# Performance work log

Measured on AMD Instinct MI355X. Metric: run time of the kernel, lower is better.

## Reference

```python
import jax, jax.numpy as jnp
import numpy as np

# Static module config (from init_kwargs)
N, C, H, W = 2, 256, 64, 64
S = 2            # scale_factor
K = 5            # up_kernel
G = 1            # up_group
CC = 64          # compressed_channels
EK = 3           # encoder_kernel
HOUT, WOUT = H * S, W * S


def conv2d(x, w, b, pad):
    y = jax.lax.conv_general_dilated(
        x, w, window_strides=(1, 1), padding=[(pad, pad), (pad, pad)],
        dimension_numbers=('NCHW', 'OIHW', 'NCHW'))
    return y + b[None, :, None, None]


def grid_sample_border(img, gx, gy):
    """Bilinear grid_sample, padding_mode='border', align_corners=True.
    img: (N, Cm, Hh, Ww); gx, gy: (N, Hout, Wout) normalized coords in [-1,1]."""
    Hh, Ww = img.shape[2], img.shape[3]
    ix = jnp.clip((gx + 1.0) * 0.5 * (Ww - 1), 0.0, Ww - 1)
    iy = jnp.clip((gy + 1.0) * 0.5 * (Hh - 1), 0.0, Hh - 1)
    x0 = jnp.floor(ix)
    y0 = jnp.floor(iy)
    fx = ix - x0
    fy = iy - y0
    x0i = x0.astype(jnp.int32)
    y0i = y0.astype(jnp.int32)
    x1i = jnp.minimum(x0i + 1, Ww - 1)
    y1i = jnp.minimum(y0i + 1, Hh - 1)

    def per_n(im, x0n, x1n, y0n, y1n, fxn, fyn):
        v00 = im[:, y0n, x0n]   # (Cm, Hout, Wout)
        v01 = im[:, y0n, x1n]
        v10 = im[:, y1n, x0n]
        v11 = im[:, y1n, x1n]
        return (v00 * (1 - fxn) * (1 - fyn) + v01 * fxn * (1 - fyn)
                + v10 * (1 - fxn) * fyn + v11 * fxn * fyn)

    return jax.vmap(per_n)(img, x0i, x1i, y0i, y1i, fx, fy)


def setup_inputs() -> dict:
    key = jax.random.key(0)
    ks = jax.random.split(key, 8)
    x = jax.random.normal(ks[0], (N, C, H, W), dtype=jnp.float32)
    w_comp = jax.random.normal(ks[1], (CC, C, 1, 1), dtype=jnp.float32) * 0.05
    b_comp = jax.random.normal(ks[2], (CC,), dtype=jnp.float32) * 0.01
    # conv_offset is zero-init in the original; use small random weights to
    # exercise the deformable path.
    w_off = jax.random.normal(ks[3], (G * 2 * S * S, CC, EK, EK), dtype=jnp.float32) * 0.01
    b_off = jax.random.normal(ks[4], (G * 2 * S * S,), dtype=jnp.float32) * 0.01
    w_ker = jax.random.normal(ks[5], (K * K * G, CC, EK, EK), dtype=jnp.float32) * 0.01
    b_ker = jax.random.normal(ks[6], (K * K * G,), dtype=jnp.float32) * 0.01
    return {'x': x, 'w_comp': w_comp, 'b_comp': b_comp,
            'w_off': w_off, 'b_off': b_off, 'w_ker': w_ker, 'b_ker': b_ker}


def reference(x, w_comp, b_comp, w_off, b_off, w_ker, b_ker):
    # 1) channel compressor (1x1 conv)
    comp = conv2d(x, w_comp, b_comp, 0)                      # (N, CC, H, W)
    # 2) offset + kernel prediction (3x3 convs)
    off = conv2d(comp, w_off, b_off, (EK - 1) // 2)          # (N, 2*S*S*G, H, W)
    ker = conv2d(comp, w_ker, b_ker, (EK - 1) // 2)          # (N, G*K*K, H, W)
    # 3) kernel space normalizer: softmax over K*K per group
    m = ker.reshape(N, G, K * K, H, W)
    m = jax.nn.softmax(m, axis=2).reshape(N, G * K * K, H, W)
    # 4) kernel space expander: pixel_shuffle offset -> (N,2,HOUT,WOUT)
    o = off.reshape(N, 2, S, S, H, W).transpose(0, 1, 4, 2, 5, 3).reshape(N, 2, HOUT, WOUT)
    ox = o[:, 0] * (2.0 / (W - 1))   # x offset, normalized
    oy = o[:, 1] * (2.0 / (H - 1))   # y offset, normalized
    base_y = jnp.repeat(jnp.linspace(-1.0, 1.0, H), S)       # (HOUT,)
    base_x = jnp.repeat(jnp.linspace(-1.0, 1.0, W), S)       # (WOUT,)
    gx = base_x[None, None, :] + ox                          # (N, HOUT, WOUT)
    gy = base_y[None, :, None] + oy
    mask_up = grid_sample_border(m, gx, gy)                  # (N, G*K*K, HOUT, WOUT)
    # 5) CARAFE reassembly: unfold features at low res, weighted sum.
    pad = (K - 1) // 2
    xp = jnp.pad(x, ((0, 0), (0, 0), (pad, pad), (pad, pad)))
    unf = jnp.stack([xp[:, :, i:i + H, j:j + W]
                     for i in range(K) for j in range(K)], axis=2)  # (N,C,K*K,H,W)
    Cg = C // G
    unf = unf.reshape(N, G, Cg, K * K, H, W)
    # mask[..., h*S+p, w*S+q] selects low-res position (h, w): reshape instead
    # of materializing the (N,G,Cg,K*K,HOUT,WOUT) gathered tensor.
    mr = mask_up.reshape(N, G, K * K, H, S, W, S)
    out = jnp.einsum('ngckhw,ngkhpwq->ngchpwq', unf, mr)
    return out.reshape(N, C, HOUT, WOUT)
```

## Files before the change

### kernel.cpp

```cpp
#include <hip/hip_runtime.h>

#define NB 2
#define CIN 256
#define HH 64
#define WW 64
#define CCMP 64
#define HO 128
#define WO 128

#define CPLD 66
#define CPCH (CPLD * CPLD)
#define CPIMG (CCMP * CPCH)
#define CPTOT (NB * CPIMG)

#define OFF_OFFB  (CPTOT)
#define OFF_KERB  (OFF_OFFB + 65536)
#define OFF_WTS   (OFF_KERB + 204800)

__global__ __launch_bounds__(256) void k1_comp(const float* __restrict__ x,
                                               const float* __restrict__ wc,
                                               const float* __restrict__ bc,
                                               float* __restrict__ comp_pad) {
  int b = blockIdx.x;
  int n = b >> 8;
  int ccg = (b >> 4) & 15;
  int hq = b & 15;
  int hsub = threadIdx.x >> 6;
  int w = threadIdx.x & 63;
  int h = hq * 4 + hsub;

  float acc[4];
#pragma unroll
  for (int j = 0; j < 4; ++j) acc[j] = bc[ccg * 4 + j];
  const float* xp = x + ((size_t)(n * CIN) * HH + h) * WW + w;
#pragma unroll 4
  for (int c = 0; c < CIN; ++c) {
    float xv = xp[(size_t)c * HH * WW];
#pragma unroll
    for (int j = 0; j < 4; ++j) acc[j] += xv * wc[(ccg * 4 + j) * CIN + c];
  }
  float* plane = comp_pad + (size_t)n * CPIMG + (size_t)(ccg * 4) * CPCH;
#pragma unroll
  for (int j = 0; j < 4; ++j)
    plane[(size_t)j * CPCH + (h + 1) * CPLD + (w + 1)] = acc[j];

  if (threadIdx.x < 32) {
    int ch = threadIdx.x >> 3;
    int rw = (threadIdx.x >> 1) & 3;
    int side = threadIdx.x & 1;
    plane[(size_t)ch * CPCH + (hq * 4 + rw + 1) * CPLD + side * 65] = 0.f;
  }
  if (hq == 0)
    for (int i = threadIdx.x; i < 4 * CPLD; i += 256)
      plane[(size_t)(i / CPLD) * CPCH + (i % CPLD)] = 0.f;
  if (hq == 15)
    for (int i = threadIdx.x; i < 4 * CPLD; i += 256)
      plane[(size_t)(i / CPLD) * CPCH + 65 * CPLD + (i % CPLD)] = 0.f;
}

__global__ __launch_bounds__(256) void k2_conv3(const float* __restrict__ comp_pad,
                                                const float* __restrict__ w_off,
                                                const float* __restrict__ b_off,
                                                const float* __restrict__ w_ker,
                                                const float* __restrict__ b_ker,
                                                float* __restrict__ offb,
                                                float* __restrict__ kerb) {
  int b = blockIdx.x;
  int n = b / (17 * 16);
  int r = b % (17 * 16);
  int ocp = r / 16;
  int hq = r % 16;
  int hsub = threadIdx.x >> 6;
  int w = threadIdx.x & 63;
  int h = hq * 4 + hsub;

  int oc0 = ocp * 2;
  int oc1 = (oc0 + 1 < 33) ? oc0 + 1 : 32;
  const float* wp0 = (oc0 < 8) ? (w_off + (size_t)oc0 * CCMP * 9)
                               : (w_ker + (size_t)(oc0 - 8) * CCMP * 9);
  const float* wp1 = (oc1 < 8) ? (w_off + (size_t)oc1 * CCMP * 9)
                               : (w_ker + (size_t)(oc1 - 8) * CCMP * 9);
  float a0 = (oc0 < 8) ? b_off[oc0] : b_ker[oc0 - 8];
  float a1 = (oc1 < 8) ? b_off[oc1] : b_ker[oc1 - 8];

  const float* base = comp_pad + (size_t)n * CPIMG + h * CPLD + w;

  for (int cb = 0; cb < CCMP; cb += 4) {
    float t[4][9];
#pragma unroll
    for (int cc = 0; cc < 4; ++cc) {
      const float* p = base + (size_t)(cb + cc) * CPCH;
#pragma unroll
      for (int dy = 0; dy < 3; ++dy)
#pragma unroll
        for (int dx = 0; dx < 3; ++dx)
          t[cc][dy * 3 + dx] = p[dy * CPLD + dx];
    }
#pragma unroll
    for (int cc = 0; cc < 4; ++cc)
#pragma unroll
      for (int k = 0; k < 9; ++k) {
        float tv = t[cc][k];
        a0 += tv * wp0[(cb + cc) * 9 + k];
        a1 += tv * wp1[(cb + cc) * 9 + k];
      }
  }

  int pos = h * WW + w;
  if (oc0 < 8) offb[(size_t)(n * 8 + oc0) * 4096 + pos] = a0;
  else         kerb[(size_t)(n * 25 + (oc0 - 8)) * 4096 + pos] = a0;
  if (oc1 < 8) offb[(size_t)(n * 8 + oc1) * 4096 + pos] = a1;
  else         kerb[(size_t)(n * 25 + (oc1 - 8)) * 4096 + pos] = a1;
}

__global__ __launch_bounds__(64, 2) void k34_wts(const float* __restrict__ offb,
                                                 const float* __restrict__ kerb,
                                                 float* __restrict__ wts) {
  int t = blockIdx.x * 64 + threadIdx.x;
  int n = t >> 14;
  int r = t & 16383;
  int ho = r >> 7;
  int wo = r & 127;
  int h = ho >> 1, p = ho & 1, w = wo >> 1, q = wo & 1;
  int pq = p * 2 + q;
  float offx = offb[((size_t)(n * 8 + pq) * HH + h) * WW + w];
  float offy = offb[((size_t)(n * 8 + 4 + pq) * HH + h) * WW + w];
  float ix = fminf(fmaxf((float)w + offx, 0.f), 63.f);
  float iy = fminf(fmaxf((float)h + offy, 0.f), 63.f);
  float x0f = floorf(ix), y0f = floorf(iy);
  float fx = ix - x0f, fy = iy - y0f;
  int x0 = (int)x0f, y0 = (int)y0f;
  int x1 = min(x0 + 1, 63), y1 = min(y0 + 1, 63);
  float g0 = (1.f - fx) * (1.f - fy), g1 = fx * (1.f - fy);
  float g2 = (1.f - fx) * fy,         g3 = fx * fy;

  const float* mb = kerb + (size_t)n * 25 * 4096;
  int c0 = y0 * 64 + x0, c1 = y0 * 64 + x1, c2 = y1 * 64 + x0, c3 = y1 * 64 + x1;

  float v0[25], v1[25], v2[25], v3[25];
#pragma unroll
  for (int k = 0; k < 25; ++k) {
    const float* mk = mb + (size_t)k * 4096;
    v0[k] = mk[c0]; v1[k] = mk[c1]; v2[k] = mk[c2]; v3[k] = mk[c3];
  }
  float m0 = v0[0], m1 = v1[0], m2 = v2[0], m3 = v3[0];
#pragma unroll
  for (int k = 1; k < 25; ++k) {
    m0 = fmaxf(m0, v0[k]); m1 = fmaxf(m1, v1[k]);
    m2 = fmaxf(m2, v2[k]); m3 = fmaxf(m3, v3[k]);
  }
  float S0 = 0.f, S1 = 0.f, S2 = 0.f, S3 = 0.f;
#pragma unroll
  for (int k = 0; k < 25; ++k) {
    v0[k] = expf(v0[k] - m0); S0 += v0[k];
    v1[k] = expf(v1[k] - m1); S1 += v1[k];
    v2[k] = expf(v2[k] - m2); S2 += v2[k];
    v3[k] = expf(v3[k] - m3); S3 += v3[k];
  }
  float f0 = g0 / S0, f1 = g1 / S1, f2 = g2 / S2, f3 = g3 / S3;

  float* wp = wts + (((size_t)(n * HH + h) * 4 + pq) * 25) * 64 + w;
#pragma unroll
  for (int k = 0; k < 25; ++k)
    wp[k * 64] = v0[k] * f0 + v1[k] * f1 + v2[k] * f2 + v3[k] * f3;
}

__global__ __launch_bounds__(256, 2) void k5_out(const float* __restrict__ x,
                                                 const float* __restrict__ wts,
                                                 float* __restrict__ out) {
  int b = blockIdx.x;
  int n = b >> 9;
  int r = b & 511;
  int h = r >> 3;
  int cg = r & 7;
  int wave = threadIdx.x >> 6;
  int w = threadIdx.x & 63;
  int c0 = cg * 32 + wave * 8;

  const float* wbase = wts + (size_t)(n * HH + h) * 100 * 64 + w;
  float wt[100];
#pragma unroll
  for (int i = 0; i < 100; ++i) wt[i] = wbase[i * 64];

  for (int ci = 0; ci < 8; ++ci) {
    int c = c0 + ci;
    const float* xc = x + (size_t)(n * CIN + c) * HH * WW;
    float a0 = 0.f, a1 = 0.f, a2 = 0.f, a3 = 0.f;
#pragma unroll
    for (int dy = 0; dy < 5; ++dy) {
      int rr = h + dy - 2;
      bool rok = (unsigned)rr < (unsigned)HH;
      const float* xr = xc + rr * WW;
#pragma unroll
      for (int dx = 0; dx < 5; ++dx) {
        int cc = w + dx - 2;
        float xv = (rok && (unsigned)cc < (unsigned)WW) ? xr[cc] : 0.f;
        int k = dy * 5 + dx;
        a0 += wt[k] * xv;
        a1 += wt[25 + k] * xv;
        a2 += wt[50 + k] * xv;
        a3 += wt[75 + k] * xv;
      }
    }
    float* o0 = out + ((size_t)(n * CIN + c) * HO + 2 * h) * WO + 2 * w;
    *(float2*)o0 = make_float2(a0, a1);
    *(float2*)(o0 + WO) = make_float2(a2, a3);
  }
}

extern "C" void kernel_launch(void* const* d_in, const int* in_sizes, int n_in,
                              void* d_out, int out_size, void* d_ws, size_t ws_size,
                              hipStream_t stream) {
  const float* x      = (const float*)d_in[0];
  const float* w_comp = (const float*)d_in[1];
  const float* b_comp = (const float*)d_in[2];
  const float* w_off  = (const float*)d_in[3];
  const float* b_off  = (const float*)d_in[4];
  const float* w_ker  = (const float*)d_in[5];
  const float* b_ker  = (const float*)d_in[6];
  float* out = (float*)d_out;

  float* ws       = (float*)d_ws;
  float* comp_pad = ws;
  float* offb     = ws + OFF_OFFB;
  float* kerb     = ws + OFF_KERB;
  float* wts      = ws + OFF_WTS;

  k1_comp<<<512, 256, 0, stream>>>(x, w_comp, b_comp, comp_pad);
  k2_conv3<<<544, 256, 0, stream>>>(comp_pad, w_off, b_off, w_ker, b_ker, offb, kerb);
  k34_wts<<<512, 64, 0, stream>>>(offb, kerb, wts);
  k5_out<<<1024, 256, 0, stream>>>(x, wts, out);
}
```

Measured before the change: 73.39 us.

## Pre-pad input for reassembly, widen compression channel tiling, raise k5 occupancy

Adds a kernel that copies x into a zero-padded 68x68-per-plane buffer, so the reassembly kernel can read its 5x5 window without bounds checks or predicated loads. The compression 1x1 conv now computes 8 output channels per thread instead of 4, halving the block count and the re-reads of x. k5's launch bounds now ask for 3 blocks per SM. The cost is an extra kernel launch plus a full extra read and write of x (about 9.5 MB of padded traffic), and tighter register limits in k5 with its 100-float weight array, which may cause spills.

```diff
diff --git a/kernel.cpp b/kernel.cpp
--- a/kernel.cpp
+++ b/kernel.cpp
@@ -13,48 +13,67 @@
 #define CPIMG (CCMP * CPCH)
 #define CPTOT (NB * CPIMG)
 
+#define XPLD 68
+#define XPCH (XPLD * XPLD)
+#define XPIMG (CIN * XPCH)
+#define XPTOT (NB * XPIMG)
+
 #define OFF_OFFB  (CPTOT)
 #define OFF_KERB  (OFF_OFFB + 65536)
 #define OFF_WTS   (OFF_KERB + 204800)
+#define OFF_XPAD  (OFF_WTS + 819200)
+
+__global__ __launch_bounds__(256) void k0x_pad(const float* __restrict__ x,
+                                               float* __restrict__ xpad) {
+  int plane = blockIdx.x;
+  const float* xs = x + (size_t)plane * HH * WW;
+  float* xd = xpad + (size_t)plane * XPCH;
+  for (int i = threadIdx.x; i < XPCH; i += 256) {
+    int hp = i / XPLD, wp = i % XPLD;
+    int h = hp - 2, w = wp - 2;
+    bool ok = ((unsigned)h < (unsigned)HH) && ((unsigned)w < (unsigned)WW);
+    xd[i] = ok ? xs[h * WW + w] : 0.f;
+  }
+}
 
 __global__ __launch_bounds__(256) void k1_comp(const float* __restrict__ x,
                                                const float* __restrict__ wc,
                                                const float* __restrict__ bc,
                                                float* __restrict__ comp_pad) {
   int b = blockIdx.x;
-  int n = b >> 8;
-  int ccg = (b >> 4) & 15;
+  int n = b >> 7;
+  int ccg = (b >> 4) & 7;
   int hq = b & 15;
   int hsub = threadIdx.x >> 6;
   int w = threadIdx.x & 63;
   int h = hq * 4 + hsub;
 
-  float acc[4];
-#pragma unroll
-  for (int j = 0; j < 4; ++j) acc[j] = bc[ccg * 4 + j];
+  float acc[8];
+#pragma unroll
+  for (int j = 0; j < 8; ++j) acc[j] = bc[ccg * 8 + j];
   const float* xp = x + ((size_t)(n * CIN) * HH + h) * WW + w;
 #pragma unroll 4
   for (int c = 0; c < CIN; ++c) {
     float xv = xp[(size_t)c * HH * WW];
 #pragma unroll
-    for (int j = 0; j < 4; ++j) acc[j] += xv * wc[(ccg * 4 + j) * CIN + c];
-  }
-  float* plane = comp_pad + (size_t)n * CPIMG + (size_t)(ccg * 4) * CPCH;
-#pragma unroll
-  for (int j = 0; j < 4; ++j)
+    for (int j = 0; j < 8; ++j) acc[j] += xv * wc[(ccg * 8 + j) * CIN + c];
+  }
+  float* plane = comp_pad + (size_t)n * CPIMG + (size_t)(ccg * 8) * CPCH;
+#pragma unroll
+  for (int j = 0; j < 8; ++j)
     plane[(size_t)j * CPCH + (h + 1) * CPLD + (w + 1)] = acc[j];
 
-  if (threadIdx.x < 32) {
+  if (threadIdx.x < 64) {
     int ch = threadIdx.x >> 3;
     int rw = (threadIdx.x >> 1) & 3;
     int side = threadIdx.x & 1;
     plane[(size_t)ch * CPCH + (hq * 4 + rw + 1) * CPLD + side * 65] = 0.f;
   }
   if (hq == 0)
-    for (int i = threadIdx.x; i < 4 * CPLD; i += 256)
+    for (int i = threadIdx.x; i < 8 * CPLD; i += 256)
       plane[(size_t)(i / CPLD) * CPCH + (i % CPLD)] = 0.f;
   if (hq == 15)
-    for (int i = threadIdx.x; i < 4 * CPLD; i += 256)
+    for (int i = threadIdx.x; i < 8 * CPLD; i += 256)
       plane[(size_t)(i / CPLD) * CPCH + 65 * CPLD + (i % CPLD)] = 0.f;
 }
 
@@ -165,7 +184,7 @@
     wp[k * 64] = v0[k] * f0 + v1[k] * f1 + v2[k] * f2 + v3[k] * f3;
 }
 
-__global__ __launch_bounds__(256, 2) void k5_out(const float* __restrict__ x,
+__global__ __launch_bounds__(256, 3) void k5_out(const float* __restrict__ xpad,
                                                  const float* __restrict__ wts,
                                                  float* __restrict__ out) {
   int b = blockIdx.x;
@@ -184,17 +203,14 @@
 
   for (int ci = 0; ci < 8; ++ci) {
     int c = c0 + ci;
-    const float* xc = x + (size_t)(n * CIN + c) * HH * WW;
+    const float* xc = xpad + (size_t)(n * CIN + c) * XPCH + h * XPLD + w;
     float a0 = 0.f, a1 = 0.f, a2 = 0.f, a3 = 0.f;
 #pragma unroll
     for (int dy = 0; dy < 5; ++dy) {
-      int rr = h + dy - 2;
-      bool rok = (unsigned)rr < (unsigned)HH;
-      const float* xr = xc + rr * WW;
+      const float* xr = xc + dy * XPLD;
 #pragma unroll
       for (int dx = 0; dx < 5; ++dx) {
-        int cc = w + dx - 2;
-        float xv = (rok && (unsigned)cc < (unsigned)WW) ? xr[cc] : 0.f;
+        float xv = xr[dx];
         int k = dy * 5 + dx;
         a0 += wt[k] * xv;
         a1 += wt[25 + k] * xv;
@@ -225,9 +241,11 @@
   float* offb     = ws + OFF_OFFB;
   float* kerb     = ws + OFF_KERB;
   float* wts      = ws + OFF_WTS;
-
-  k1_comp<<<512, 256, 0, stream>>>(x, w_comp, b_comp, comp_pad);
+  float* xpad     = ws + OFF_XPAD;
+
+  k0x_pad<<<NB * CIN, 256, 0, stream>>>(x, xpad);
+  k1_comp<<<256, 256, 0, stream>>>(x, w_comp, b_comp, comp_pad);
   k2_conv3<<<544, 256, 0, stream>>>(comp_pad, w_off, b_off, w_ker, b_ker, offb, kerb);
   k34_wts<<<512, 64, 0, stream>>>(offb, kerb, wts);
-  k5_out<<<1024, 256, 0, stream>>>(x, wts, out);
-}
+  k5_out<<<1024, 256, 0, stream>>>(xpad, wts, out);
+}
```

Result: slower. 89.59 us (+22.1%).

## Fuse mask-weight computation into CARAFE output kernel via shared memory

Applied to the files above, without the earlier changes.

Merges the softmax/bilinear weight kernel into the reassembly kernel. Each 512-thread block first computes the 100x64 weight tile for one row into shared memory, then all waves read it into registers and process 16 channels each. This removes one launch and the global round trip of the weights buffer. In exchange only half the threads work during the weight phase, the grid shrinks to 256 blocks, and each of the two channel-half blocks for a row recomputes the same weights.

```diff
diff --git a/kernel.cpp b/kernel.cpp
--- a/kernel.cpp
+++ b/kernel.cpp
@@ -15,7 +15,6 @@
 
 #define OFF_OFFB  (CPTOT)
 #define OFF_KERB  (OFF_OFFB + 65536)
-#define OFF_WTS   (OFF_KERB + 204800)
 
 __global__ __launch_bounds__(256) void k1_comp(const float* __restrict__ x,
                                                const float* __restrict__ wc,
@@ -113,77 +112,69 @@
   else         kerb[(size_t)(n * 25 + (oc1 - 8)) * 4096 + pos] = a1;
 }
 
-__global__ __launch_bounds__(64, 2) void k34_wts(const float* __restrict__ offb,
-                                                 const float* __restrict__ kerb,
-                                                 float* __restrict__ wts) {
-  int t = blockIdx.x * 64 + threadIdx.x;
-  int n = t >> 14;
-  int r = t & 16383;
-  int ho = r >> 7;
-  int wo = r & 127;
-  int h = ho >> 1, p = ho & 1, w = wo >> 1, q = wo & 1;
-  int pq = p * 2 + q;
-  float offx = offb[((size_t)(n * 8 + pq) * HH + h) * WW + w];
-  float offy = offb[((size_t)(n * 8 + 4 + pq) * HH + h) * WW + w];
-  float ix = fminf(fmaxf((float)w + offx, 0.f), 63.f);
-  float iy = fminf(fmaxf((float)h + offy, 0.f), 63.f);
-  float x0f = floorf(ix), y0f = floorf(iy);
-  float fx = ix - x0f, fy = iy - y0f;
-  int x0 = (int)x0f, y0 = (int)y0f;
-  int x1 = min(x0 + 1, 63), y1 = min(y0 + 1, 63);
-  float g0 = (1.f - fx) * (1.f - fy), g1 = fx * (1.f - fy);
-  float g2 = (1.f - fx) * fy,         g3 = fx * fy;
-
-  const float* mb = kerb + (size_t)n * 25 * 4096;
-  int c0 = y0 * 64 + x0, c1 = y0 * 64 + x1, c2 = y1 * 64 + x0, c3 = y1 * 64 + x1;
-
-  float v0[25], v1[25], v2[25], v3[25];
-#pragma unroll
-  for (int k = 0; k < 25; ++k) {
-    const float* mk = mb + (size_t)k * 4096;
-    v0[k] = mk[c0]; v1[k] = mk[c1]; v2[k] = mk[c2]; v3[k] = mk[c3];
-  }
-  float m0 = v0[0], m1 = v1[0], m2 = v2[0], m3 = v3[0];
-#pragma unroll
-  for (int k = 1; k < 25; ++k) {
-    m0 = fmaxf(m0, v0[k]); m1 = fmaxf(m1, v1[k]);
-    m2 = fmaxf(m2, v2[k]); m3 = fmaxf(m3, v3[k]);
-  }
-  float S0 = 0.f, S1 = 0.f, S2 = 0.f, S3 = 0.f;
-#pragma unroll
-  for (int k = 0; k < 25; ++k) {
-    v0[k] = expf(v0[k] - m0); S0 += v0[k];
-    v1[k] = expf(v1[k] - m1); S1 += v1[k];
-    v2[k] = expf(v2[k] - m2); S2 += v2[k];
-    v3[k] = expf(v3[k] - m3); S3 += v3[k];
-  }
-  float f0 = g0 / S0, f1 = g1 / S1, f2 = g2 / S2, f3 = g3 / S3;
-
-  float* wp = wts + (((size_t)(n * HH + h) * 4 + pq) * 25) * 64 + w;
-#pragma unroll
-  for (int k = 0; k < 25; ++k)
-    wp[k * 64] = v0[k] * f0 + v1[k] * f1 + v2[k] * f2 + v3[k] * f3;
-}
-
-__global__ __launch_bounds__(256, 2) void k5_out(const float* __restrict__ x,
-                                                 const float* __restrict__ wts,
-                                                 float* __restrict__ out) {
+__global__ __launch_bounds__(512) void k345(const float* __restrict__ x,
+                                            const float* __restrict__ offb,
+                                            const float* __restrict__ kerb,
+                                            float* __restrict__ out) {
+  __shared__ float wl[100][64];
   int b = blockIdx.x;
-  int n = b >> 9;
-  int r = b & 511;
-  int h = r >> 3;
-  int cg = r & 7;
-  int wave = threadIdx.x >> 6;
-  int w = threadIdx.x & 63;
-  int c0 = cg * 32 + wave * 8;
-
-  const float* wbase = wts + (size_t)(n * HH + h) * 100 * 64 + w;
+  int n = b >> 7;
+  int h = (b >> 1) & 63;
+  int cg2 = b & 1;
+  int tid = threadIdx.x;
+
+  if (tid < 256) {
+    int w = tid & 63, pq = tid >> 6;
+    float offx = offb[((size_t)(n * 8 + pq) * HH + h) * WW + w];
+    float offy = offb[((size_t)(n * 8 + 4 + pq) * HH + h) * WW + w];
+    float ix = fminf(fmaxf((float)w + offx, 0.f), 63.f);
+    float iy = fminf(fmaxf((float)h + offy, 0.f), 63.f);
+    float x0f = floorf(ix), y0f = floorf(iy);
+    float fx = ix - x0f, fy = iy - y0f;
+    int x0 = (int)x0f, y0 = (int)y0f;
+    int x1 = min(x0 + 1, 63), y1 = min(y0 + 1, 63);
+    float g0 = (1.f - fx) * (1.f - fy), g1 = fx * (1.f - fy);
+    float g2 = (1.f - fx) * fy,         g3 = fx * fy;
+
+    const float* mb = kerb + (size_t)n * 25 * 4096;
+    int c0 = y0 * 64 + x0, c1 = y0 * 64 + x1, c2 = y1 * 64 + x0, c3 = y1 * 64 + x1;
+
+    float v0[25], v1[25], v2[25], v3[25];
+#pragma unroll
+    for (int k = 0; k < 25; ++k) {
+      const float* mk = mb + (size_t)k * 4096;
+      v0[k] = mk[c0]; v1[k] = mk[c1]; v2[k] = mk[c2]; v3[k] = mk[c3];
+    }
+    float m0 = v0[0], m1 = v1[0], m2 = v2[0], m3 = v3[0];
+#pragma unroll
+    for (int k = 1; k < 25; ++k) {
+      m0 = fmaxf(m0, v0[k]); m1 = fmaxf(m1, v1[k]);
+      m2 = fmaxf(m2, v2[k]); m3 = fmaxf(m3, v3[k]);
+    }
+    float S0 = 0.f, S1 = 0.f, S2 = 0.f, S3 = 0.f;
+#pragma unroll
+    for (int k = 0; k < 25; ++k) {
+      v0[k] = expf(v0[k] - m0); S0 += v0[k];
+      v1[k] = expf(v1[k] - m1); S1 += v1[k];
+      v2[k] = expf(v2[k] - m2); S2 += v2[k];
+      v3[k] = expf(v3[k] - m3); S3 += v3[k];
+    }
+    float f0 = g0 / S0, f1 = g1 / S1, f2 = g2 / S2, f3 = g3 / S3;
+#pragma unroll
+    for (int k = 0; k < 25; ++k)
+      wl[pq * 25 + k][w] = v0[k] * f0 + v1[k] * f1 + v2[k] * f2 + v3[k] * f3;
+  }
+  __syncthreads();
+
+  int wave = tid >> 6;
+  int w = tid & 63;
   float wt[100];
 #pragma unroll
-  for (int i = 0; i < 100; ++i) wt[i] = wbase[i * 64];
-
-  for (int ci = 0; ci < 8; ++ci) {
-    int c = c0 + ci;
+  for (int i = 0; i < 100; ++i) wt[i] = wl[i][w];
+
+  int ch0 = cg2 * 128 + wave * 16;
+  for (int ci = 0; ci < 16; ++ci) {
+    int c = ch0 + ci;
     const float* xc = x + (size_t)(n * CIN + c) * HH * WW;
     float a0 = 0.f, a1 = 0.f, a2 = 0.f, a3 = 0.f;
 #pragma unroll
@@ -224,10 +215,8 @@
   float* comp_pad = ws;
   float* offb     = ws + OFF_OFFB;
   float* kerb     = ws + OFF_KERB;
-  float* wts      = ws + OFF_WTS;
 
   k1_comp<<<512, 256, 0, stream>>>(x, w_comp, b_comp, comp_pad);
   k2_conv3<<<544, 256, 0, stream>>>(comp_pad, w_off, b_off, w_ker, b_ker, offb, kerb);
-  k34_wts<<<512, 64, 0, stream>>>(offb, kerb, wts);
-  k5_out<<<1024, 256, 0, stream>>>(x, wts, out);
-}
+  k345<<<256, 512, 0, stream>>>(x, offb, kerb, out);
+}
```

Result: faster. 70.86 us (-3.5%).

## Transpose input to padded NHWC and restructure reassembly with channel-parallel lanes

Applied to the files above, without the earlier changes.

Adds a kernel that transposes x into a zero-padded NHWC workspace buffer, so the reassembly kernel can map lanes to channels and read coalesced rows without bounds checks. The weights buffer is switched to a per-position layout, and each block now walks 8 output positions with weights loaded as wave-uniform values instead of holding 100 weights per thread in registers. The cost is an extra kernel launch and a full transpose of x through memory. Output stores now hit strided channel planes, two floats per lane, which may coalesce poorly.

```diff
diff --git a/kernel.cpp b/kernel.cpp
--- a/kernel.cpp
+++ b/kernel.cpp
@@ -13,9 +13,56 @@
 #define CPIMG (CCMP * CPCH)
 #define CPTOT (NB * CPIMG)
 
+#define XTROW 256
+#define XTLINE (68 * XTROW)
+#define XTIMG (68 * XTLINE)
+#define XTTOT (NB * XTIMG)
+
 #define OFF_OFFB  (CPTOT)
 #define OFF_KERB  (OFF_OFFB + 65536)
 #define OFF_WTS   (OFF_KERB + 204800)
+#define OFF_XTP   (OFF_WTS + 819200)
+
+__global__ __launch_bounds__(256) void k0t(const float* __restrict__ x,
+                                           float* __restrict__ xTp) {
+  int b = blockIdx.x;
+  int n = b / 68;
+  int hp = b % 68;
+  float* dst = xTp + (size_t)n * XTIMG + (size_t)hp * XTLINE;
+  if (hp < 2 || hp >= 66) {
+    for (int i = threadIdx.x; i < XTLINE; i += 256) dst[i] = 0.f;
+    return;
+  }
+  int h = hp - 2;
+  __shared__ float tile[64][65];
+  int w = threadIdx.x & 63;
+  int cs = threadIdx.x >> 6;
+  const float* src = x + (size_t)n * CIN * 4096 + h * 64 + w;
+
+  for (int p = 0; p < 4; ++p) {
+    int cb = p * 64;
+#pragma unroll
+    for (int ci = 0; ci < 16; ++ci) {
+      int cl = cs * 16 + ci;
+      tile[cl][w] = src[(size_t)(cb + cl) * 4096];
+    }
+    __syncthreads();
+    int cl = threadIdx.x & 63;
+    int wsb = threadIdx.x >> 6;
+#pragma unroll
+    for (int wi = 0; wi < 16; ++wi) {
+      int ww = wsb * 16 + wi;
+      dst[(size_t)(ww + 2) * XTROW + cb + cl] = tile[cl][ww];
+    }
+    __syncthreads();
+  }
+  for (int i = threadIdx.x; i < 4 * 256; i += 256) {
+    int wq = i >> 8;
+    int c = i & 255;
+    int wcol = (wq < 2) ? wq : 64 + wq;
+    dst[(size_t)wcol * XTROW + c] = 0.f;
+  }
+}
 
 __global__ __launch_bounds__(256) void k1_comp(const float* __restrict__ x,
                                                const float* __restrict__ wc,
@@ -159,52 +206,44 @@
   }
   float f0 = g0 / S0, f1 = g1 / S1, f2 = g2 / S2, f3 = g3 / S3;
 
-  float* wp = wts + (((size_t)(n * HH + h) * 4 + pq) * 25) * 64 + w;
+  float* wp = wts + ((size_t)((n * HH + h) * WW) + w) * 100 + pq * 25;
 #pragma unroll
   for (int k = 0; k < 25; ++k)
-    wp[k * 64] = v0[k] * f0 + v1[k] * f1 + v2[k] * f2 + v3[k] * f3;
-}
-
-__global__ __launch_bounds__(256, 2) void k5_out(const float* __restrict__ x,
-                                                 const float* __restrict__ wts,
-                                                 float* __restrict__ out) {
+    wp[k] = v0[k] * f0 + v1[k] * f1 + v2[k] * f2 + v3[k] * f3;
+}
+
+__global__ __launch_bounds__(256) void k5_nhwc(const float* __restrict__ xTp,
+                                               const float* __restrict__ wts,
+                                               float* __restrict__ out) {
   int b = blockIdx.x;
   int n = b >> 9;
-  int r = b & 511;
-  int h = r >> 3;
-  int cg = r & 7;
+  int h = (b >> 3) & 63;
+  int wseg = b & 7;
   int wave = threadIdx.x >> 6;
-  int w = threadIdx.x & 63;
-  int c0 = cg * 32 + wave * 8;
-
-  const float* wbase = wts + (size_t)(n * HH + h) * 100 * 64 + w;
-  float wt[100];
-#pragma unroll
-  for (int i = 0; i < 100; ++i) wt[i] = wbase[i * 64];
-
-  for (int ci = 0; ci < 8; ++ci) {
-    int c = c0 + ci;
-    const float* xc = x + (size_t)(n * CIN + c) * HH * WW;
+  int lane = threadIdx.x & 63;
+  int c = wave * 64 + lane;
+  const float* xbase = xTp + (size_t)n * XTIMG;
+
+  for (int pos = 0; pos < 8; ++pos) {
+    int w = wseg * 8 + pos;
+    const float* wp = wts + ((size_t)((n * HH + h) * WW) + w) * 100;
     float a0 = 0.f, a1 = 0.f, a2 = 0.f, a3 = 0.f;
 #pragma unroll
     for (int dy = 0; dy < 5; ++dy) {
-      int rr = h + dy - 2;
-      bool rok = (unsigned)rr < (unsigned)HH;
-      const float* xr = xc + rr * WW;
+      const float* xr = xbase + ((size_t)(h + dy) * 68 + w) * XTROW + c;
 #pragma unroll
       for (int dx = 0; dx < 5; ++dx) {
-        int cc = w + dx - 2;
-        float xv = (rok && (unsigned)cc < (unsigned)WW) ? xr[cc] : 0.f;
+        float xv = xr[dx * XTROW];
         int k = dy * 5 + dx;
-        a0 += wt[k] * xv;
-        a1 += wt[25 + k] * xv;
-        a2 += wt[50 + k] * xv;
-        a3 += wt[75 + k] * xv;
+        a0 += wp[k] * xv;
+        a1 += wp[25 + k] * xv;
+        a2 += wp[50 + k] * xv;
+        a3 += wp[75 + k] * xv;
       }
     }
-    float* o0 = out + ((size_t)(n * CIN + c) * HO + 2 * h) * WO + 2 * w;
-    *(float2*)o0 = make_float2(a0, a1);
-    *(float2*)(o0 + WO) = make_float2(a2, a3);
+    float* o = out + ((size_t)(n * CIN + c) * HO + 2 * h) * WO + 2 * w;
+    *(float2*)o = make_float2(a0, a1);
+    *(float2*)(o + WO) = make_float2(a2, a3);
   }
 }
 
@@ -225,9 +264,11 @@
   float* offb     = ws + OFF_OFFB;
   float* kerb     = ws + OFF_KERB;
   float* wts      = ws + OFF_WTS;
-
+  float* xTp      = ws + OFF_XTP;
+
+  k0t<<<NB * 68, 256, 0, stream>>>(x, xTp);
   k1_comp<<<512, 256, 0, stream>>>(x, w_comp, b_comp, comp_pad);
   k2_conv3<<<544, 256, 0, stream>>>(comp_pad, w_off, b_off, w_ker, b_ker, offb, kerb);
   k34_wts<<<512, 64, 0, stream>>>(offb, kerb, wts);
-  k5_out<<<1024, 256, 0, stream>>>(x, wts, out);
-}
+  k5_nhwc<<<1024, 256, 0, stream>>>(xTp, wts, out);
+}
```

Result: slower. 115.3 us (+57.1%).
